# Kernel tuning notes

Hardware: AMD Instinct MI355X
Metric: run time of the kernel (lower is better)

## Reference

```python
import jax, jax.numpy as jnp
import numpy as np

B, C, P, L = 128, 5, 5, 5
D = 128
USER_NUM, TITLE_NUM, ENTITY_NUM, REL_NUM = 50000, 30000, 100000, 100


def setup_inputs() -> dict:
    key = jax.random.key(0)
    k = jax.random.split(key, 22)
    f = jnp.float32
    s = 0.1  # weight scale to keep LSTM gates in a sane range
    return {
        "candidate_newsindex": jax.random.randint(k[0], (B, C), 0, TITLE_NUM),
        "user_index": jax.random.randint(k[1], (B,), 0, USER_NUM),
        "total_paths_index": jax.random.randint(k[2], (USER_NUM, C, P, L), 0, TITLE_NUM),
        "total_type_index": jax.random.randint(k[3], (USER_NUM, C, P, L), 0, 3),
        "total_relations_index": jax.random.randint(k[4], (USER_NUM, C, P, L), 0, REL_NUM),
        "entity_emb": jax.random.normal(k[5], (ENTITY_NUM, D), f),
        "relation_emb": jax.random.normal(k[6], (REL_NUM, D), f),
        "user_emb": jax.random.normal(k[7], (USER_NUM, D), f),
        "news_emb": jax.random.normal(k[8], (TITLE_NUM, D), f),
        "type_emb": jax.random.normal(k[9], (3, D), f),
        "Wih0": jax.random.normal(k[10], (P, 4 * D, 3 * D), f) * s,
        "Whh0": jax.random.normal(k[11], (P, 4 * D, D), f) * s,
        "bih0": jax.random.normal(k[12], (P, 4 * D), f) * s,
        "bhh0": jax.random.normal(k[13], (P, 4 * D), f) * s,
        "Wih1": jax.random.normal(k[14], (P, 4 * D, D), f) * s,
        "Whh1": jax.random.normal(k[15], (P, 4 * D, D), f) * s,
        "bih1": jax.random.normal(k[16], (P, 4 * D), f) * s,
        "bhh1": jax.random.normal(k[17], (P, 4 * D), f) * s,
        "W1": jax.random.normal(k[18], (16, D), f) * s,
        "b1": jax.random.normal(k[19], (16,), f) * s,
        "W2": jax.random.normal(k[20], (1, 16), f) * s,
        "b2": jax.random.normal(k[21], (1,), f) * s,
    }


def _lstm2(x, Wih0, Whh0, bih0, bhh0, Wih1, Whh1, bih1, bhh1):
    """2-layer PyTorch-style LSTM (gate order i,f,g,o). x: [N, T, in] -> [N, T, H]."""
    def layer(x, Wih, Whh, bih, bhh):
        N = x.shape[0]
        H = Whh.shape[1]
        h0 = jnp.zeros((N, H), x.dtype)
        c0 = jnp.zeros((N, H), x.dtype)
        b = bih + bhh
        def step(carry, xt):
            h, c = carry
            g = xt @ Wih.T + h @ Whh.T + b
            i, f, gg, o = jnp.split(g, 4, axis=-1)
            c = jax.nn.sigmoid(f) * c + jax.nn.sigmoid(i) * jnp.tanh(gg)
            h = jax.nn.sigmoid(o) * jnp.tanh(c)
            return (h, c), h
        _, ys = jax.lax.scan(step, (h0, c0), x.swapaxes(0, 1))
        return ys.swapaxes(0, 1)
    x = layer(x, Wih0, Whh0, bih0, bhh0)
    x = layer(x, Wih1, Whh1, bih1, bhh1)
    return x


def reference(candidate_newsindex, user_index, total_paths_index, total_type_index,
              total_relations_index, entity_emb, relation_emb, user_emb, news_emb,
              type_emb, Wih0, Whh0, bih0, bhh0, Wih1, Whh1, bih1, bhh1,
              W1, b1, W2, b2):
    bpath = total_paths_index[user_index]  # [B,C,P,L]
    btype = total_type_index[user_index]
    brel = total_relations_index[user_index]
    # per-node embedding selected by type: 0->user, 1->news, else entity
    node = jnp.where((btype == 0)[..., None], user_emb[bpath],
                     jnp.where((btype == 1)[..., None], news_emb[bpath], entity_emb[bpath]))
    inp = jnp.concatenate([node, type_emb[btype], relation_emb[brel]], axis=-1)  # [B,C,P,L,3D]
    Bb, Cc, Pp, Ll, F = inp.shape
    x = inp.transpose(2, 0, 1, 3, 4).reshape(Pp, Bb * Cc, Ll, F)  # per-path batches
    outs = jax.vmap(_lstm2)(x, Wih0, Whh0, bih0, bhh0, Wih1, Whh1, bih1, bhh1)  # [P,BC,L,H]
    idx = jnp.arange(Pp)
    sel = outs[idx, :, idx, :]  # LSTM i's output at timestep i -> [P, BC, H]
    ps = jax.nn.sigmoid(jnp.maximum(sel @ W1.T + b1, 0.0) @ W2.T + b2)[..., 0]  # [P,BC]
    ps_mean = ps.reshape(Pp, Bb, Cc).mean(axis=0)  # [B,C]
    # faithful to source: total_output accumulates over candidates j, so the score
    # for candidate j is the cumulative mean of path scores for candidates 0..j
    total_score = jnp.cumsum(ps_mean, axis=1) / jnp.arange(1, Cc + 1, dtype=ps_mean.dtype)
    emb_score = jax.nn.sigmoid(jnp.sum(news_emb[candidate_newsindex] * user_emb[user_index][:, None, :], axis=-1))
    return emb_score + total_score
```

## Files before the change

kernel.cpp:

```cpp
#include <hip/hip_runtime.h>
#include <math.h>

#define BB   128
#define CC   5
#define PP   5
#define LL   5
#define DD   128
#define NSEQ 640
#define GATES 512
#define IN0  384
#define HPAD 136

typedef __attribute__((ext_vector_type(8))) short short8;
typedef __attribute__((ext_vector_type(4))) float f32x4;

__device__ __forceinline__ float sigf(float x){ return 1.0f/(1.0f+__expf(-x)); }
__device__ __forceinline__ float tanhfast(float x){ return 1.0f - 2.0f/(__expf(2.0f*x)+1.0f); }

__device__ __forceinline__ unsigned short f2bf(float x){
    union { float f; unsigned u; } v; v.f = x;
    unsigned r = v.u + 0x7FFF + ((v.u >> 16) & 1);
    return (unsigned short)(r >> 16);
}

__device__ __constant__ int c_ptmap[15] = {0,5,6,10,11,12,15,16,17,18,20,21,22,23,24};

__global__ void stage0_kernel(const float* __restrict__ Wih0, const float* __restrict__ Whh0,
                              const float* __restrict__ Wih1, const float* __restrict__ Whh1,
                              const float* __restrict__ bih0, const float* __restrict__ bhh0,
                              const float* __restrict__ bih1, const float* __restrict__ bhh1,
                              unsigned short* __restrict__ F0, unsigned short* __restrict__ F1,
                              unsigned short* __restrict__ F2, unsigned short* __restrict__ F3,
                              float* __restrict__ b0, float* __restrict__ b1c,
                              float* __restrict__ psum,
                              const int* __restrict__ user_index,
                              const int* __restrict__ tpath, const int* __restrict__ ttype,
                              const int* __restrict__ trel,
                              const float* __restrict__ entity_emb, const float* __restrict__ relation_emb,
                              const float* __restrict__ user_emb, const float* __restrict__ news_emb,
                              const float* __restrict__ type_emb,
                              unsigned short* __restrict__ X){
    int bx = blockIdx.x;
    if (bx < 985){
        int id = bx*256 + threadIdx.x;
        const int NF0 = PP*12*32*64;
        const int NFH = PP*4*32*64;
        if (id < NF0 + 3*NFH){
            const float* src; unsigned short* dst; int K, KT, fid;
            if (id < NF0){ src = Wih0; dst = F0; K = IN0; KT = 12; fid = id; }
            else {
                int j = id - NF0; int m = j / NFH; fid = j % NFH; K = DD; KT = 4;
                src = (m==0)?Whh0:(m==1)?Wih1:Whh1;
                dst = (m==0)?F1:(m==1)?F2:F3;
            }
            int lane = fid & 63; int rem = fid >> 6;
            int gt = rem & 31; rem >>= 5;
            int kt = rem % KT; int p = rem / KT;
            int g  = gt*16 + (lane & 15);
            int k0 = kt*32 + (lane >> 4)*8;
            const float* s = src + (size_t)(p*GATES + g)*K + k0;
            float4 x0 = *(const float4*)s;
            float4 x1 = *(const float4*)(s+4);
            uint4 o;
            o.x = f2bf(x0.x) | ((unsigned)f2bf(x0.y)<<16);
            o.y = f2bf(x0.z) | ((unsigned)f2bf(x0.w)<<16);
            o.z = f2bf(x1.x) | ((unsigned)f2bf(x1.y)<<16);
            o.w = f2bf(x1.z) | ((unsigned)f2bf(x1.w)<<16);
            *(uint4*)(dst + (size_t)fid*8) = o;
        } else {
            int j = id - (NF0 + 3*NFH);
            if (j < PP*GATES) b0[j] = bih0[j] + bhh0[j];
            else if (j < 2*PP*GATES){ int q = j - PP*GATES; b1c[q] = bih1[q] + bhh1[q]; }
            else if (j < 2*PP*GATES + NSEQ){ psum[j - 2*PP*GATES] = 0.0f; }
        }
    } else {
        int id = (bx - 985)*256 + threadIdx.x;
        if (id >= 15*NSEQ*48) return;
        int ptIdx = id / (NSEQ*48); int rem = id % (NSEQ*48);
        int n = rem / 48, q = rem % 48;
        int pt = c_ptmap[ptIdx];
        int p = pt / LL, t = pt % LL;
        int b = n / CC, c = n % CC;
        int u = user_index[b];
        int base = ((u*CC + c)*PP + p)*LL + t;
        int col = q*8;
        const float* s;
        if (q < 16){
            int ty = ttype[base]; int pi = tpath[base];
            const float* e = (ty==0)?user_emb:(ty==1)?news_emb:entity_emb;
            s = e + (size_t)pi*DD + col;
        } else if (q < 32){
            s = type_emb + (size_t)ttype[base]*DD + (col-128);
        } else {
            s = relation_emb + (size_t)trel[base]*DD + (col-256);
        }
        float4 x0 = *(const float4*)s, x1 = *(const float4*)(s+4);
        uint4 o;
        o.x = f2bf(x0.x) | ((unsigned)f2bf(x0.y)<<16);
        o.y = f2bf(x0.z) | ((unsigned)f2bf(x0.w)<<16);
        o.z = f2bf(x1.x) | ((unsigned)f2bf(x1.y)<<16);
        o.w = f2bf(x1.z) | ((unsigned)f2bf(x1.w)<<16);
        *(uint4*)(X + (size_t)(pt*NSEQ + n)*IN0 + col) = o;
    }
}

__global__ __launch_bounds__(256) void gemm_ih0_v5(const unsigned short* __restrict__ X,
                                                   const unsigned short* __restrict__ F0,
                                                   float* __restrict__ G0c){
    __shared__ unsigned short Bs[12*4*512];
    int bx = blockIdx.x;
    int nch = bx & 7;
    int m64 = (bx >> 3) % 10;
    int pt  = c_ptmap[bx / 80];
    int p = pt / LL;
    int tid = threadIdx.x, lane = tid & 63, w = tid >> 6;
    int r16 = lane & 15, qd = lane >> 4;

    const unsigned short* Fp = F0 + (((size_t)p*12)*32 + nch*4)*512;
    uint4 breg[12];
    #pragma unroll
    for (int j=0;j<12;j++)
        breg[j] = *(const uint4*)(Fp + (size_t)j*32*512 + tid*8);
    #pragma unroll
    for (int j=0;j<12;j++)
        *(uint4*)(Bs + j*2048 + tid*8) = breg[j];
    __syncthreads();

    f32x4 acc[4];
    #pragma unroll
    for (int i=0;i<4;i++) acc[i] = (f32x4)0.0f;
    const unsigned short* Xb = X + ((size_t)pt*NSEQ + m64*64 + w*16 + r16)*IN0 + qd*8;
    #pragma unroll
    for (int kt=0; kt<12; kt++){
        short8 a = *(const short8*)(Xb + kt*32);
        #pragma unroll
        for (int i=0;i<4;i++){
            short8 bfr = *(const short8*)(Bs + (kt*4+i)*512 + lane*8);
            acc[i] = __builtin_amdgcn_mfma_f32_16x16x32_bf16(a, bfr, acc[i], 0,0,0);
        }
    }
    int tile16 = pt*40 + m64*4 + w;
    float* dst = G0c + (((size_t)tile16*32 + nch*4)*64 + lane)*4;
    #pragma unroll
    for (int i=0;i<4;i++)
        *(f32x4*)(dst + (size_t)i*256) = acc[i];
}

__global__ __launch_bounds__(512) void lstm_v5(
    const float* __restrict__ G0c,
    const unsigned short* __restrict__ F1,
    const unsigned short* __restrict__ F2,
    const unsigned short* __restrict__ F3,
    const float* __restrict__ b0, const float* __restrict__ b1c,
    const float* __restrict__ W1, const float* __restrict__ b1v,
    const float* __restrict__ W2, const float* __restrict__ b2v,
    float* __restrict__ psum){
    __shared__ unsigned short h0T[16*HPAD];
    __shared__ unsigned short h1T[16*HPAD];
    __shared__ float h1f[16*132];
    __shared__ float mlpb[16*17];

    int p = blockIdx.x / 40, nt = blockIdx.x % 40;
    int n0 = nt*16;
    int tid = threadIdx.x;
    int lane = tid & 63, w = tid >> 6;
    int r16 = lane & 15, qd = lane >> 4;
    int j = w*16 + r16;

    short8 f2r[16], f3r[16];
    {
        const unsigned short* F2p = F2 + (size_t)p*4*32*512 + lane*8;
        const unsigned short* F3p = F3 + (size_t)p*4*32*512 + lane*8;
        #pragma unroll
        for (int kt=0; kt<4; kt++)
            #pragma unroll
            for (int i=0;i<4;i++){
                f2r[kt*4+i] = *(const short8*)(F2p + (size_t)(kt*32 + i*8 + w)*512);
                f3r[kt*4+i] = *(const short8*)(F3p + (size_t)(kt*32 + i*8 + w)*512);
            }
    }
    float bL0[4], bL1[4];
    #pragma unroll
    for (int i=0;i<4;i++){
        int col = (i*8 + w)*16 + r16;
        bL0[i] = b0[p*GATES + col];
        bL1[i] = b1c[p*GATES + col];
    }
    const unsigned short* F1p = F1 + (size_t)p*4*32*512 + lane*8;

    f32x4 pf[4];
    {
        const float* slab = G0c + (size_t)((p*LL + 0)*40 + nt)*8192;
        #pragma unroll
        for (int i=0;i<4;i++) pf[i] = *(const f32x4*)(slab + ((i*8+w)*64 + lane)*4);
    }
    float c0s[4] = {0,0,0,0}, c1s[4] = {0,0,0,0};

    for (int t=0; t<=p; t++){
        f32x4 acc[4];
        #pragma unroll
        for (int i=0;i<4;i++){
            f32x4 a = pf[i]; float bb = bL0[i];
            a[0]+=bb; a[1]+=bb; a[2]+=bb; a[3]+=bb; acc[i]=a;
        }
        if (t < p){
            const float* ns = G0c + (size_t)((p*LL + t + 1)*40 + nt)*8192;
            #pragma unroll
            for (int i=0;i<4;i++) pf[i] = *(const f32x4*)(ns + ((i*8+w)*64 + lane)*4);
        }
        if (t > 0){
            #pragma unroll
            for (int kt=0; kt<4; kt++){
                short8 a = *(const short8*)(h0T + r16*HPAD + kt*32 + qd*8);
                #pragma unroll
                for (int i=0;i<4;i++){
                    short8 bfr = *(const short8*)(F1p + (size_t)(kt*32 + i*8 + w)*512);
                    acc[i] = __builtin_amdgcn_mfma_f32_16x16x32_bf16(a, bfr, acc[i], 0,0,0);
                }
            }
        }
        __syncthreads();
        #pragma unroll
        for (int v=0; v<4; v++){
            float cc = sigf(acc[1][v])*c0s[v] + sigf(acc[0][v])*tanhfast(acc[2][v]);
            c0s[v] = cc;
            h0T[(qd*4+v)*HPAD + j] = f2bf(sigf(acc[3][v])*tanhfast(cc));
        }
        __syncthreads();
        #pragma unroll
        for (int i=0;i<4;i++){
            float bb = bL1[i];
            f32x4 a; a[0]=bb; a[1]=bb; a[2]=bb; a[3]=bb; acc[i]=a;
        }
        #pragma unroll
        for (int kt=0; kt<4; kt++){
            short8 a = *(const short8*)(h0T + r16*HPAD + kt*32 + qd*8);
            #pragma unroll
            for (int i=0;i<4;i++)
                acc[i] = __builtin_amdgcn_mfma_f32_16x16x32_bf16(a, f2r[kt*4+i], acc[i], 0,0,0);
        }
        if (t > 0){
            #pragma unroll
            for (int kt=0; kt<4; kt++){
                short8 a = *(const short8*)(h1T + r16*HPAD + kt*32 + qd*8);
                #pragma unroll
                for (int i=0;i<4;i++)
                    acc[i] = __builtin_amdgcn_mfma_f32_16x16x32_bf16(a, f3r[kt*4+i], acc[i], 0,0,0);
            }
        }
        __syncthreads();
        #pragma unroll
        for (int v=0; v<4; v++){
            float cc = sigf(acc[1][v])*c1s[v] + sigf(acc[0][v])*tanhfast(acc[2][v]);
            c1s[v] = cc;
            float hh = sigf(acc[3][v])*tanhfast(cc);
            if (t < p) h1T[(qd*4+v)*HPAD + j] = f2bf(hh);
            else       h1f[(qd*4+v)*132 + j] = hh;
        }
    }
    __syncthreads();
    if (tid < 256){
        int rr = tid & 15, hc = tid >> 4;
        const float* w1r = W1 + hc*DD;
        float acc = b1v[hc];
        #pragma unroll 4
        for (int k=0;k<DD;k++) acc = fmaf(h1f[rr*132 + k], w1r[k], acc);
        mlpb[hc*17 + rr] = fmaxf(acc, 0.0f);
    }
    __syncthreads();
    if (tid < 16){
        float s = b2v[0];
        #pragma unroll
        for (int h=0;h<16;h++) s = fmaf(mlpb[h*17 + tid], W2[h], s);
        atomicAdd(&psum[n0 + tid], 0.2f*sigf(s));
    }
}

__global__ void final_kernel(const int* __restrict__ cand, const int* __restrict__ user_index,
                             const float* __restrict__ news_emb, const float* __restrict__ user_emb,
                             const float* __restrict__ psum, float* __restrict__ out){
    int b = blockIdx.x;
    int lane = threadIdx.x;
    int u = user_index[b];
    const float* ue = user_emb + (size_t)u*DD;
    float cum = 0.0f;
    for (int c=0;c<CC;c++){
        int nb = cand[b*CC + c];
        const float* ne = news_emb + (size_t)nb*DD;
        float v = ne[lane]*ue[lane] + ne[lane+64]*ue[lane+64];
        #pragma unroll
        for (int off=32; off; off>>=1) v += __shfl_down(v, off, 64);
        if (lane == 0){
            cum += psum[b*CC + c];
            out[b*CC + c] = sigf(v) + cum/(float)(c+1);
        }
    }
}

extern "C" void kernel_launch(void* const* d_in, const int* in_sizes, int n_in,
                              void* d_out, int out_size, void* d_ws, size_t ws_size,
                              hipStream_t stream){
    const int* cand        = (const int*)d_in[0];
    const int* uidx        = (const int*)d_in[1];
    const int* tpath       = (const int*)d_in[2];
    const int* ttype       = (const int*)d_in[3];
    const int* trel        = (const int*)d_in[4];
    const float* entity_emb   = (const float*)d_in[5];
    const float* relation_emb = (const float*)d_in[6];
    const float* user_emb     = (const float*)d_in[7];
    const float* news_emb     = (const float*)d_in[8];
    const float* type_emb     = (const float*)d_in[9];
    const float* Wih0 = (const float*)d_in[10];
    const float* Whh0 = (const float*)d_in[11];
    const float* bih0 = (const float*)d_in[12];
    const float* bhh0 = (const float*)d_in[13];
    const float* Wih1 = (const float*)d_in[14];
    const float* Whh1 = (const float*)d_in[15];
    const float* bih1 = (const float*)d_in[16];
    const float* bhh1 = (const float*)d_in[17];
    const float* W1 = (const float*)d_in[18];
    const float* b1 = (const float*)d_in[19];
    const float* W2 = (const float*)d_in[20];
    const float* b2 = (const float*)d_in[21];
    float* out = (float*)d_out;

    char* ws = (char*)d_ws;
    unsigned short* F0 = (unsigned short*)ws;  ws += (size_t)PP*12*32*512*2;
    unsigned short* F1 = (unsigned short*)ws;  ws += (size_t)PP*4*32*512*2;
    unsigned short* F2 = (unsigned short*)ws;  ws += (size_t)PP*4*32*512*2;
    unsigned short* F3 = (unsigned short*)ws;  ws += (size_t)PP*4*32*512*2;
    float* b0  = (float*)ws;                   ws += PP*GATES*4;
    float* b1c = (float*)ws;                   ws += PP*GATES*4;
    unsigned short* X = (unsigned short*)ws;   ws += (size_t)PP*LL*NSEQ*IN0*2;
    float* G0c = (float*)ws;                   ws += (size_t)PP*LL*NSEQ*GATES*4;
    float* psum = (float*)ws;                  ws += NSEQ*4;

    stage0_kernel<<<985+1800,256,0,stream>>>(Wih0,Whh0,Wih1,Whh1,bih0,bhh0,bih1,bhh1,
                                             F0,F1,F2,F3,b0,b1c,psum,
                                             uidx,tpath,ttype,trel,entity_emb,relation_emb,
                                             user_emb,news_emb,type_emb,X);
    gemm_ih0_v5<<<1200,256,0,stream>>>(X, F0, G0c);
    lstm_v5<<<200,512,0,stream>>>(G0c, F1, F2, F3, b0, b1c, W1, b1, W2, b2, psum);
    final_kernel<<<BB,64,0,stream>>>(cand, uidx, news_emb, user_emb, psum, out);
}
```

Before: 233.4 us.

## Double-buffer LSTM hidden-state tiles to drop barriers, vectorize MLP head

The recurrent kernel now keeps two copies of the h0 and h1 shared-memory tiles and alternates between them by timestep parity. This removes two of the four block-wide barriers per step, because writers no longer overwrite data that other waves are still reading. The final 128-wide dot products in the small MLP use float4 loads and four independent accumulators. A `__launch_bounds__(512, 2)` hint is also added. That hint could force register spills, since the kernel keeps 32 short8 weight fragments in registers, and with only 200 blocks the extra occupancy is unlikely to be used.

Result: no change. 234.9 us (+0.6%).

```diff
diff --git a/kernel.cpp b/kernel.cpp
--- a/kernel.cpp
+++ b/kernel.cpp
@@ -146,7 +146,7 @@
         *(f32x4*)(dst + (size_t)i*256) = acc[i];
 }
 
-__global__ __launch_bounds__(512) void lstm_v5(
+__global__ __launch_bounds__(512, 2) void lstm_v6(
     const float* __restrict__ G0c,
     const unsigned short* __restrict__ F1,
     const unsigned short* __restrict__ F2,
@@ -155,8 +155,8 @@
     const float* __restrict__ W1, const float* __restrict__ b1v,
     const float* __restrict__ W2, const float* __restrict__ b2v,
     float* __restrict__ psum){
-    __shared__ unsigned short h0T[16*HPAD];
-    __shared__ unsigned short h1T[16*HPAD];
+    __shared__ unsigned short h0T[2][16*HPAD];
+    __shared__ unsigned short h1T[2][16*HPAD];
     __shared__ float h1f[16*132];
     __shared__ float mlpb[16*17];
 
@@ -197,6 +197,7 @@
     float c0s[4] = {0,0,0,0}, c1s[4] = {0,0,0,0};
 
     for (int t=0; t<=p; t++){
+        const int cur = t & 1, prv = cur ^ 1;
         f32x4 acc[4];
         #pragma unroll
         for (int i=0;i<4;i++){
@@ -211,7 +212,7 @@
         if (t > 0){
             #pragma unroll
             for (int kt=0; kt<4; kt++){
-                short8 a = *(const short8*)(h0T + r16*HPAD + kt*32 + qd*8);
+                short8 a = *(const short8*)(&h0T[prv][0] + r16*HPAD + kt*32 + qd*8);
                 #pragma unroll
                 for (int i=0;i<4;i++){
                     short8 bfr = *(const short8*)(F1p + (size_t)(kt*32 + i*8 + w)*512);
@@ -219,12 +220,11 @@
                 }
             }
         }
-        __syncthreads();
         #pragma unroll
         for (int v=0; v<4; v++){
             float cc = sigf(acc[1][v])*c0s[v] + sigf(acc[0][v])*tanhfast(acc[2][v]);
             c0s[v] = cc;
-            h0T[(qd*4+v)*HPAD + j] = f2bf(sigf(acc[3][v])*tanhfast(cc));
+            h0T[cur][(qd*4+v)*HPAD + j] = f2bf(sigf(acc[3][v])*tanhfast(cc));
         }
         __syncthreads();
         #pragma unroll
@@ -234,7 +234,7 @@
         }
         #pragma unroll
         for (int kt=0; kt<4; kt++){
-            short8 a = *(const short8*)(h0T + r16*HPAD + kt*32 + qd*8);
+            short8 a = *(const short8*)(&h0T[cur][0] + r16*HPAD + kt*32 + qd*8);
             #pragma unroll
             for (int i=0;i<4;i++)
                 acc[i] = __builtin_amdgcn_mfma_f32_16x16x32_bf16(a, f2r[kt*4+i], acc[i], 0,0,0);
@@ -242,30 +242,37 @@
         if (t > 0){
             #pragma unroll
             for (int kt=0; kt<4; kt++){
-                short8 a = *(const short8*)(h1T + r16*HPAD + kt*32 + qd*8);
+                short8 a = *(const short8*)(&h1T[prv][0] + r16*HPAD + kt*32 + qd*8);
                 #pragma unroll
                 for (int i=0;i<4;i++)
                     acc[i] = __builtin_amdgcn_mfma_f32_16x16x32_bf16(a, f3r[kt*4+i], acc[i], 0,0,0);
             }
         }
-        __syncthreads();
         #pragma unroll
         for (int v=0; v<4; v++){
             float cc = sigf(acc[1][v])*c1s[v] + sigf(acc[0][v])*tanhfast(acc[2][v]);
             c1s[v] = cc;
             float hh = sigf(acc[3][v])*tanhfast(cc);
-            if (t < p) h1T[(qd*4+v)*HPAD + j] = f2bf(hh);
+            if (t < p) h1T[cur][(qd*4+v)*HPAD + j] = f2bf(hh);
             else       h1f[(qd*4+v)*132 + j] = hh;
         }
     }
     __syncthreads();
     if (tid < 256){
         int rr = tid & 15, hc = tid >> 4;
-        const float* w1r = W1 + hc*DD;
-        float acc = b1v[hc];
-        #pragma unroll 4
-        for (int k=0;k<DD;k++) acc = fmaf(h1f[rr*132 + k], w1r[k], acc);
-        mlpb[hc*17 + rr] = fmaxf(acc, 0.0f);
+        const float4* w1r = (const float4*)(W1 + hc*DD);
+        const float4* hrow = (const float4*)(h1f + rr*132);
+        float a0 = b1v[hc], a1 = 0.0f, a2 = 0.0f, a3 = 0.0f;
+        #pragma unroll
+        for (int k=0;k<32;k++){
+            float4 wv = w1r[k];
+            float4 hv = hrow[k];
+            a0 = fmaf(hv.x, wv.x, a0);
+            a1 = fmaf(hv.y, wv.y, a1);
+            a2 = fmaf(hv.z, wv.z, a2);
+            a3 = fmaf(hv.w, wv.w, a3);
+        }
+        mlpb[hc*17 + rr] = fmaxf((a0+a1)+(a2+a3), 0.0f);
     }
     __syncthreads();
     if (tid < 16){
@@ -340,6 +347,6 @@
                                              uidx,tpath,ttype,trel,entity_emb,relation_emb,
                                              user_emb,news_emb,type_emb,X);
     gemm_ih0_v5<<<1200,256,0,stream>>>(X, F0, G0c);
-    lstm_v5<<<200,512,0,stream>>>(G0c, F1, F2, F3, b0, b1c, W1, b1, W2, b2, psum);
+    lstm_v6<<<200,512,0,stream>>>(G0c, F1, F2, F3, b0, b1c, W1, b1, W2, b2, psum);
     final_kernel<<<BB,64,0,stream>>>(cand, uidx, news_emb, user_emb, psum, out);
 }
```
